# Kernel optimization log

Measured on AMD Instinct MI355X. Metric: run time of the kernel, lower is better.

Reference implementation:

```python
import jax, jax.numpy as jnp
import numpy as np

IN, H, B, T = 64, 256, 128, 512

def _uniform(key, shape, std):
    return jax.random.uniform(key, shape, jnp.float32, -std, std)

def setup_inputs() -> dict:
    key = jax.random.key(0)
    ks = jax.random.split(key, 16)
    std = 1.0 / np.sqrt(H)
    inp = {
        'x': jax.random.normal(ks[0], (B, T, IN), jnp.float32),
        # layer 1 sLSTM cell
        'Wxh1': _uniform(ks[1], (4 * H, IN), std), 'bxh1': _uniform(ks[2], (4 * H,), std),
        'Whh1': _uniform(ks[3], (4 * H, H), std),  'bhh1': _uniform(ks[4], (4 * H,), std),
        # layer 2 sLSTM cell
        'Wxh2': _uniform(ks[5], (4 * H, H), std),  'bxh2': _uniform(ks[6], (4 * H,), std),
        'Whh2': _uniform(ks[7], (4 * H, H), std),  'bhh2': _uniform(ks[8], (4 * H,), std),
        # head MLP
        'W1': _uniform(ks[9], (H // 2, H), 1.0 / np.sqrt(H)),      'b1': _uniform(ks[10], (H // 2,), 1.0 / np.sqrt(H)),
        'W2': _uniform(ks[11], (H // 4, H // 2), 1.0 / np.sqrt(H // 2)), 'b2': _uniform(ks[12], (H // 4,), 1.0 / np.sqrt(H // 2)),
        'W3': _uniform(ks[13], (1, H // 4), 1.0 / np.sqrt(H // 4)),      'b3': _uniform(ks[14], (1,), 1.0 / np.sqrt(H // 4)),
    }
    return inp

def _slstm_cell(x, h, c, m, n, Wxh, bxh, Whh, bhh):
    # gates: [B, 4H]
    gates = x @ Wxh.T + bxh + h @ Whh.T + bhh
    ig, fg, zg, og = jnp.split(gates, 4, axis=1)
    z_t = jnp.tanh(zg)
    o_t = jax.nn.sigmoid(og)
    # stabilizer: log(exp(fg)) = fg, log(exp(ig)) = ig
    m_t = jnp.maximum(fg + m, ig)
    i_t = jnp.exp(ig - m_t)
    f_t = jnp.exp(fg + m - m_t)
    c_t = f_t * c + i_t * z_t
    n_t = f_t * n + i_t
    h_t = o_t * (c_t / n_t)
    return h_t, c_t, m_t, n_t

def reference(x, Wxh1, bxh1, Whh1, bhh1, Wxh2, bxh2, Whh2, bhh2, W1, b1, W2, b2, W3, b3):
    Bq = x.shape[0]
    z = jnp.zeros((Bq, H), x.dtype)
    init = (z, z, z, z, z, z, z, z)  # (h1,c1,m1,n1,h2,c2,m2,n2)

    def step(carry, x_t):
        h1, c1, m1, n1, h2, c2, m2, n2 = carry
        h1, c1, m1, n1 = _slstm_cell(x_t, h1, c1, m1, n1, Wxh1, bxh1, Whh1, bhh1)
        h2, c2, m2, n2 = _slstm_cell(h1, h2, c2, m2, n2, Wxh2, bxh2, Whh2, bhh2)
        return (h1, c1, m1, n1, h2, c2, m2, n2), None

    carry, _ = jax.lax.scan(step, init, jnp.swapaxes(x, 0, 1))  # scan over time
    out = carry[4]  # last h2 == outputs[:, -1, :]
    out = jax.nn.relu(out @ W1.T + b1)   # dropout is identity in eval
    out = jax.nn.relu(out @ W2.T + b2)
    out = out @ W3.T + b3
    return out.squeeze(-1)  # [B]
```

## Files before the change

### kernel.cpp

```cpp
#include <hip/hip_runtime.h>
#include <stdint.h>

typedef unsigned short ushort_t;
typedef __attribute__((ext_vector_type(8))) short short8;
typedef __attribute__((ext_vector_type(4))) float float4v;
typedef __attribute__((ext_vector_type(4))) int int4v;

#define TSTEPS 512
#define NBATCH 128
#define HID 256
#define NIN 64
#define RB 32
#define NBHID (NBATCH*HID)

#define OFF_FLAGS   0u
#define OFF_BIAS    4096u
#define OFF_H1R     16384u
#define RING_BYTES  (RB*2u*NBATCH*HID*2u)
#define OFF_H2R     (OFF_H1R + RING_BYTES)
#define OFF_WF1     (OFF_H2R + RING_BYTES)
#define WF1_FRAGS   (16*8*4*4)
#define OFF_WF2     (OFF_WF1 + WF1_FRAGS*1024u)
#define WF2_FRAGS   (16*8*6*4)
#define OFF_HOUT    (OFF_WF2 + WF2_FRAGS*1024u)

__device__ __forceinline__ ushort_t bf16h(float f) {
    unsigned u = __float_as_uint(f);
    u += 0x7fffu + ((u >> 16) & 1u);
    return (ushort_t)(u >> 16);
}
__device__ __forceinline__ float bf16f(ushort_t h) {
    return __uint_as_float(((unsigned)h) << 16);
}


__device__ __forceinline__ int ld_cg_i32(const void* p) {
    int r;
    asm volatile("global_load_dword %0, %1, off sc0 sc1\n\ts_waitcnt vmcnt(0)"
                 : "=v"(r) : "v"(p) : "memory");
    return r;
}
__device__ __forceinline__ float ld_cg_f32(const void* p) {
    float r;
    asm volatile("global_load_dword %0, %1, off sc0 sc1\n\ts_waitcnt vmcnt(0)"
                 : "=v"(r) : "v"(p) : "memory");
    return r;
}
__device__ __forceinline__ void ld_cg_x2(int4v& a, int4v& b, const void* pa, const void* pb) {
    asm volatile("global_load_dwordx4 %0, %2, off sc0 sc1\n\t"
                 "global_load_dwordx4 %1, %3, off sc0 sc1\n\t"
                 "s_waitcnt vmcnt(0)"
                 : "=&v"(a), "=&v"(b)
                 : "v"(pa), "v"(pb) : "memory");
}
__device__ __forceinline__ void ld_cg_x4(int4v& a, int4v& b, int4v& c, int4v& d,
                                         const void* pa, const void* pb,
                                         const void* pc, const void* pd) {
    asm volatile("global_load_dwordx4 %0, %4, off sc0 sc1\n\t"
                 "global_load_dwordx4 %1, %5, off sc0 sc1\n\t"
                 "global_load_dwordx4 %2, %6, off sc0 sc1\n\t"
                 "global_load_dwordx4 %3, %7, off sc0 sc1\n\t"
                 "s_waitcnt vmcnt(0)"
                 : "=&v"(a), "=&v"(b), "=&v"(c), "=&v"(d)
                 : "v"(pa), "v"(pb), "v"(pc), "v"(pd) : "memory");
}
__device__ __forceinline__ void st_cg_u16(void* p, unsigned v) {
    asm volatile("global_store_short %0, %1, off sc0 sc1" :: "v"(p), "v"(v) : "memory");
}
__device__ __forceinline__ void st_cg_f32(void* p, float v) {
    asm volatile("global_store_dword %0, %1, off sc0 sc1" :: "v"(p), "v"(v) : "memory");
}
__device__ __forceinline__ void flag_release(void* p, int v) {
    asm volatile("s_waitcnt vmcnt(0)\n\tglobal_store_dword %0, %1, off sc0 sc1"
                 :: "v"(p), "v"(v) : "memory");
}


__global__ void prep_misc(const float* bxh1, const float* bhh1,
                          const float* bxh2, const float* bhh2,
                          float* bias, int* flags, ushort_t* h1r, ushort_t* h2r)
{
    int n = blockIdx.x * blockDim.x + threadIdx.x;
    if (n < 1024)       bias[n] = bxh1[n] + bhh1[n];
    else if (n < 2048)  bias[n] = bxh2[n - 1024] + bhh2[n - 1024];
    else if (n < 2304)  flags[n - 2048] = 0;
    else if (n < 2304 + 65536)  h1r[(RB-1)*2*NBHID + (n - 2304)] = 0;
    else if (n < 2304 + 131072) h2r[(RB-1)*2*NBHID + (n - 2304 - 65536)] = 0;
}

__global__ void prep_wf(const float* Wxh1, const float* Whh1,
                        const float* Wxh2, const float* Whh2,
                        ushort_t* wf1, ushort_t* wf2)
{
    int n = blockIdx.x * blockDim.x + threadIdx.x;
    const int L1E = WF1_FRAGS * 512;
    const int L2E = WF2_FRAGS * 512;
    if (n >= L1E + L2E) return;
    int layer = (n >= L1E) ? 1 : 0;
    int e = layer ? (n - L1E) : n;
    int el = e & 511;
    int f  = e >> 9;
    int lane = el >> 3, j = el & 7;
    int nt = f & 3;
    int rem = f >> 2;
    int i, wv, slice, F, S;
    if (!layer) { F = 4; S = 10; i = rem & 3; wv = (rem >> 2) & 7; slice = rem >> 5; }
    else        { F = 6; S = 16; i = rem % 6; int r2 = rem / 6; wv = r2 & 7; slice = r2 >> 3; }
    int fg = wv * F + i;
    int col = lane & 15;
    int row = nt * 256 + slice * 16 + col;
    float val = 0.f;
    if (fg < 3 * S) {
        int sec = (fg < S) ? 0 : ((fg < 2 * S) ? 1 : 2);
        int ks = (fg - sec * S) * 32 + (lane >> 4) * 8 + j;
        float w;
        if (!layer) w = (ks < 256) ? Whh1[row * 256 + ks] : Wxh1[row * 64 + (ks - 256)];
        else        w = (ks < 256) ? Wxh2[row * 256 + ks] : Whh2[row * 256 + (ks - 256)];
        ushort_t hi = bf16h(w);
        val = (sec < 2) ? bf16f(hi) : (w - bf16f(hi));
    }
    (layer ? wf2 : wf1)[e] = bf16h(val);
}


template<int LAYER, int F, int S, int PITCH>
__device__ __forceinline__ void run_layer(
    int g, int slice, int tid, const float* __restrict__ x,
    int* flags, const float* bias,
    ushort_t* h1r, ushort_t* h2r, const ushort_t* wfrag, float* hOut,
    ushort_t* sA, ushort_t* sB, float (*red)[4][64][4])
{
    const int wv = tid >> 6, lane = tid & 63;
    const int mrow = lane & 15, q = lane >> 4;
    int* f1 = flags + g * 16;
    int* f2 = flags + 128 + g * 16;
    int* myflag = flags + LAYER * 128 + g * 16 + slice;

    short8 bw[4][F];
    {
        const ushort_t* base = wfrag + (size_t)((slice * 8 + wv) * F) * 4 * 512;
        #pragma unroll
        for (int i = 0; i < F; i++)
            #pragma unroll
            for (int nt = 0; nt < 4; nt++)
                bw[nt][i] = *(const short8*)(base + (i * 4 + nt) * 512 + lane * 8);
    }

    float bs[4];
    #pragma unroll
    for (int nt = 0; nt < 4; nt++)
        bs[nt] = bias[LAYER * 1024 + nt * 256 + slice * 16 + mrow];

    float cst[4] = {0,0,0,0}, mst[4] = {0,0,0,0}, nst[4] = {0,0,0,0};

    for (int t = 0; t < TSTEPS; t++) {
        if (LAYER == 0 && tid >= 128 && tid < 256) {
            int idx = tid - 128;
            int r = idx >> 3, o = idx & 7;
            const float* xsrc = x + ((size_t)(g * 16 + r) * TSTEPS + t) * NIN + o * 8;
            float4v x0 = *(const float4v*)xsrc;
            float4v x1 = *(const float4v*)(xsrc + 4);
            float xs[8] = {x0[0], x0[1], x0[2], x0[3], x1[0], x1[1], x1[2], x1[3]};
            union { ushort_t u[8]; int4v v4; } hiP, loP;
            #pragma unroll
            for (int z = 0; z < 8; z++) {
                ushort_t hi = bf16h(xs[z]);
                hiP.u[z] = hi;
                loP.u[z] = bf16h(xs[z] - bf16f(hi));
            }
            *(int4v*)(sA + r * PITCH + (32 + o) * 8) = hiP.v4;
            *(int4v*)(sB + r * PITCH + (32 + o) * 8) = loP.v4;
        }

        if (tid < 64) {
            int* p = nullptr; int thr = 0;
            if (LAYER == 0) {
                if (lane < 16)      { p = f1 + lane;        thr = t; }
                else if (lane < 32) { p = f2 + (lane - 16); thr = t - 30; }
            } else {
                if (lane < 16)      { p = f1 + lane;        thr = t + 1; }
                else if (lane < 32) { p = f2 + (lane - 16); thr = t; }
            }
            if (p)
                while (ld_cg_i32(p) < thr) { }
        }
        __syncthreads();

        {
            int r = tid >> 5, k = tid & 31;
            int row = g * 16 + r;
            if (LAYER == 0) {
                int slot = (t - 1) & (RB - 1);
                const ushort_t* base = h1r + (size_t)slot * 2 * NBHID + (size_t)row * HID;
                const void* p0 = base + k * 8;
                const void* p1 = base + (size_t)NBHID + k * 8;
                int4v d0, d1;
                ld_cg_x2(d0, d1, p0, p1);
                *(int4v*)(sA + r * PITCH + k * 8) = d0;
                *(int4v*)(sB + r * PITCH + k * 8) = d1;
            } else {
                int s1 = t & (RB - 1), s2 = (t - 1) & (RB - 1);
                const ushort_t* b1h = h1r + (size_t)s1 * 2 * NBHID + (size_t)row * HID;
                const ushort_t* b2h = h2r + (size_t)s2 * 2 * NBHID + (size_t)row * HID;
                const void* p0 = b1h + k * 8;
                const void* p1 = b2h + k * 8;
                const void* p2 = b1h + (size_t)NBHID + k * 8;
                const void* p3 = b2h + (size_t)NBHID + k * 8;
                int4v d0, d1, d2, d3;
                ld_cg_x4(d0, d1, d2, d3, p0, p1, p2, p3);
                *(int4v*)(sA + r * PITCH + k * 8)        = d0;
                *(int4v*)(sA + r * PITCH + (32 + k) * 8) = d1;
                *(int4v*)(sB + r * PITCH + k * 8)        = d2;
                *(int4v*)(sB + r * PITCH + (32 + k) * 8) = d3;
            }
        }
        __syncthreads();

        float4v acc[4] = {};
        #pragma unroll
        for (int i = 0; i < F; i++) {
            const int fg = wv * F + i;
            short8 a;
            if (fg < 3 * S) {
                int sec = (fg >= S && fg < 2 * S) ? 1 : 0;
                int ks = ((fg < S) ? fg : ((fg < 2 * S) ? fg - S : fg - 2 * S)) * 32;
                const ushort_t* ap = (sec ? sB : sA) + mrow * PITCH + ks + q * 8;
                a = *(const short8*)ap;
            } else {
                a = (short8){0,0,0,0,0,0,0,0};
            }
            #pragma unroll
            for (int nt = 0; nt < 4; nt++)
                acc[nt] = __builtin_amdgcn_mfma_f32_16x16x32_bf16(a, bw[nt][i], acc[nt], 0, 0, 0);
        }

        if (wv >= 4) {
            #pragma unroll
            for (int nt = 0; nt < 4; nt++) *(float4v*)red[wv][nt][lane] = acc[nt];
        }
        __syncthreads();
        if (wv < 4) {
            #pragma unroll
            for (int nt = 0; nt < 4; nt++) acc[nt] += *(const float4v*)red[wv + 4][nt][lane];
            if (wv >= 2) {
                #pragma unroll
                for (int nt = 0; nt < 4; nt++) *(float4v*)red[wv][nt][lane] = acc[nt];
            }
        }
        __syncthreads();
        if (wv < 2) {
            #pragma unroll
            for (int nt = 0; nt < 4; nt++) acc[nt] += *(const float4v*)red[wv + 2][nt][lane];
            if (wv == 1) {
                #pragma unroll
                for (int nt = 0; nt < 4; nt++) *(float4v*)red[1][nt][lane] = acc[nt];
            }
        }
        __syncthreads();

        if (wv == 0) {
            #pragma unroll
            for (int nt = 0; nt < 4; nt++) acc[nt] += *(const float4v*)red[1][nt][lane];

            ushort_t* ring = LAYER ? h2r : h1r;
            int slotW = t & (RB - 1);
            #pragma unroll
            for (int r = 0; r < 4; r++) {
                float ig  = acc[0][r] + bs[0];
                float fgt = acc[1][r] + bs[1];
                float zg  = acc[2][r] + bs[2];
                float og  = acc[3][r] + bs[3];
                float zc = fminf(fmaxf(zg, -15.f), 15.f);
                float e2 = __expf(2.f * zc);
                float zt = (e2 - 1.f) / (e2 + 1.f);
                float ot = 1.f / (1.f + __expf(-og));
                float mt = fmaxf(fgt + mst[r], ig);
                float it = __expf(ig - mt);
                float ft = __expf(fgt + mst[r] - mt);
                cst[r] = ft * cst[r] + it * zt;
                nst[r] = ft * nst[r] + it;
                mst[r] = mt;
                float h = ot * (cst[r] / nst[r]);
                ushort_t hi = bf16h(h);
                ushort_t lo = bf16h(h - bf16f(hi));
                int row = g * 16 + q * 4 + r;
                int col = slice * 16 + mrow;
                st_cg_u16(ring + ((size_t)(slotW * 2 + 0) * NBATCH + row) * HID + col, (unsigned)hi);
                st_cg_u16(ring + ((size_t)(slotW * 2 + 1) * NBATCH + row) * HID + col, (unsigned)lo);
                if (LAYER == 1 && t == TSTEPS - 1)
                    st_cg_f32(hOut + (size_t)row * HID + col, h);
            }
            if (lane == 0)
                flag_release(myflag, t + 1);
        }
    }
}

__global__ __launch_bounds__(512, 2) void recur(
    const float* __restrict__ x,
    int* flags, const float* bias,
    ushort_t* h1r, ushort_t* h2r, const ushort_t* wf1, const ushort_t* wf2, float* hOut)
{
    __shared__ ushort_t sA[16 * 520];
    __shared__ ushort_t sB[16 * 520];
    __shared__ float red[8][4][64][4];
    int g = blockIdx.x & 7;
    int loc = blockIdx.x >> 3;
    if (loc < 16)
        run_layer<0, 4, 10, 328>(g, loc, threadIdx.x, x, flags, bias, h1r, h2r, wf1, hOut, sA, sB, red);
    else
        run_layer<1, 6, 16, 520>(g, loc - 16, threadIdx.x, x, flags, bias, h1r, h2r, wf2, hOut, sA, sB, red);
}


__global__ void head_mlp(const float* hOut, const float* W1, const float* b1,
                         const float* W2, const float* b2, const float* W3, const float* b3,
                         float* out)
{
    __shared__ float h[256];
    __shared__ float a1[128];
    __shared__ float a2[64];
    int b = blockIdx.x, j = threadIdx.x;
    for (int k = j; k < 256; k += 128)
        h[k] = ld_cg_f32(hOut + (size_t)b * HID + k);
    __syncthreads();
    float s = b1[j];
    for (int k = 0; k < 256; k++) s += W1[j * 256 + k] * h[k];
    a1[j] = fmaxf(s, 0.f);
    __syncthreads();
    if (j < 64) {
        float s2 = b2[j];
        for (int k = 0; k < 128; k++) s2 += W2[j * 128 + k] * a1[k];
        a2[j] = fmaxf(s2, 0.f);
    }
    __syncthreads();
    if (j == 0) {
        float s3 = b3[0];
        for (int k = 0; k < 64; k++) s3 += W3[k] * a2[k];
        out[b] = s3;
    }
}


extern "C" void kernel_launch(void* const* d_in, const int* in_sizes, int n_in,
                              void* d_out, int out_size, void* d_ws, size_t ws_size,
                              hipStream_t stream)
{
    const float* x    = (const float*)d_in[0];
    const float* Wxh1 = (const float*)d_in[1];
    const float* bxh1 = (const float*)d_in[2];
    const float* Whh1 = (const float*)d_in[3];
    const float* bhh1 = (const float*)d_in[4];
    const float* Wxh2 = (const float*)d_in[5];
    const float* bxh2 = (const float*)d_in[6];
    const float* Whh2 = (const float*)d_in[7];
    const float* bhh2 = (const float*)d_in[8];
    const float* W1   = (const float*)d_in[9];
    const float* b1   = (const float*)d_in[10];
    const float* W2   = (const float*)d_in[11];
    const float* b2   = (const float*)d_in[12];
    const float* W3   = (const float*)d_in[13];
    const float* b3   = (const float*)d_in[14];

    char* w = (char*)d_ws;
    int*      flags = (int*)(w + OFF_FLAGS);
    float*    bias  = (float*)(w + OFF_BIAS);
    ushort_t* h1r   = (ushort_t*)(w + OFF_H1R);
    ushort_t* h2r   = (ushort_t*)(w + OFF_H2R);
    ushort_t* wf1   = (ushort_t*)(w + OFF_WF1);
    ushort_t* wf2   = (ushort_t*)(w + OFF_WF2);
    float*    hOut  = (float*)(w + OFF_HOUT);

    prep_misc<<<(2304 + 131072 + 255) / 256, 256, 0, stream>>>(bxh1, bhh1, bxh2, bhh2,
                                                               bias, flags, h1r, h2r);
    prep_wf<<<((WF1_FRAGS + WF2_FRAGS) * 512 + 255) / 256, 256, 0, stream>>>(
        Wxh1, Whh1, Wxh2, Whh2, wf1, wf2);

    const float* xp = x;
    void* args[] = { (void*)&xp, (void*)&flags, (void*)&bias,
                     (void*)&h1r, (void*)&h2r, (void*)&wf1, (void*)&wf2, (void*)&hOut };
    hipLaunchCooperativeKernel((void*)recur, dim3(256), dim3(512), args, 0, stream);

    head_mlp<<<NBATCH, 128, 0, stream>>>(hOut, W1, b1, W2, b2, W3, b3, (float*)d_out);
}
```

Before: 1.983 ms.

## Replace per-step flag handshakes with generation-tagged ring entries

```diff
diff --git a/kernel.cpp b/kernel.cpp
--- a/kernel.cpp
+++ b/kernel.cpp
@@ -12,17 +12,19 @@
 #define NIN 64
 #define RB 32
 #define NBHID (NBATCH*HID)
+#define RING_DW (RB*NBHID)
 
 #define OFF_FLAGS   0u
 #define OFF_BIAS    4096u
 #define OFF_H1R     16384u
-#define RING_BYTES  (RB*2u*NBATCH*HID*2u)
+#define RING_BYTES  (RB*(unsigned)NBATCH*HID*4u)
 #define OFF_H2R     (OFF_H1R + RING_BYTES)
 #define OFF_WF1     (OFF_H2R + RING_BYTES)
 #define WF1_FRAGS   (16*8*4*4)
 #define OFF_WF2     (OFF_WF1 + WF1_FRAGS*1024u)
 #define WF2_FRAGS   (16*8*6*4)
 #define OFF_HOUT    (OFF_WF2 + WF2_FRAGS*1024u)
+
 
 __device__ __forceinline__ ushort_t bf16h(float f) {
     unsigned u = __float_as_uint(f);
@@ -64,28 +66,55 @@
                  : "=&v"(a), "=&v"(b), "=&v"(c), "=&v"(d)
                  : "v"(pa), "v"(pb), "v"(pc), "v"(pd) : "memory");
 }
-__device__ __forceinline__ void st_cg_u16(void* p, unsigned v) {
-    asm volatile("global_store_short %0, %1, off sc0 sc1" :: "v"(p), "v"(v) : "memory");
+__device__ __forceinline__ void st_cg_u32(void* p, unsigned v) {
+    asm volatile("global_store_dword %0, %1, off sc0 sc1" :: "v"(p), "v"(v) : "memory");
+}
+__device__ __forceinline__ void st_cg_i32(int* p, int v) {
+    asm volatile("global_store_dword %0, %1, off sc0 sc1" :: "v"(p), "v"(v) : "memory");
 }
 __device__ __forceinline__ void st_cg_f32(void* p, float v) {
     asm volatile("global_store_dword %0, %1, off sc0 sc1" :: "v"(p), "v"(v) : "memory");
 }
-__device__ __forceinline__ void flag_release(void* p, int v) {
-    asm volatile("s_waitcnt vmcnt(0)\n\tglobal_store_dword %0, %1, off sc0 sc1"
-                 :: "v"(p), "v"(v) : "memory");
+
+__device__ __forceinline__ bool tags8_ok(int4v a, int4v b, unsigned eg) {
+    return (((unsigned)a[0] & 31u) == eg) & (((unsigned)a[1] & 31u) == eg) &
+           (((unsigned)a[2] & 31u) == eg) & (((unsigned)a[3] & 31u) == eg) &
+           (((unsigned)b[0] & 31u) == eg) & (((unsigned)b[1] & 31u) == eg) &
+           (((unsigned)b[2] & 31u) == eg) & (((unsigned)b[3] & 31u) == eg);
+}
+
+__device__ __forceinline__ void emit_hilo8(int4v d0, int4v d1, ushort_t* pA, ushort_t* pB) {
+    union { ushort_t u[8]; int4v v4; } hiP, loP;
+    #pragma unroll
+    for (int z = 0; z < 8; z++) {
+        unsigned u = ((unsigned)(z < 4 ? d0[z] : d1[z - 4])) & ~31u;
+        float f = __uint_as_float(u);
+        ushort_t hi = bf16h(f);
+        hiP.u[z] = hi;
+        loP.u[z] = bf16h(f - bf16f(hi));
+    }
+    *(int4v*)pA = hiP.v4;
+    *(int4v*)pB = loP.v4;
 }
 
 
 __global__ void prep_misc(const float* bxh1, const float* bhh1,
                           const float* bxh2, const float* bhh2,
-                          float* bias, int* flags, ushort_t* h1r, ushort_t* h2r)
+                          float* bias, int* flags, unsigned* h1r, unsigned* h2r)
 {
     int n = blockIdx.x * blockDim.x + threadIdx.x;
     if (n < 1024)       bias[n] = bxh1[n] + bhh1[n];
     else if (n < 2048)  bias[n] = bxh2[n - 1024] + bhh2[n - 1024];
     else if (n < 2304)  flags[n - 2048] = 0;
-    else if (n < 2304 + 65536)  h1r[(RB-1)*2*NBHID + (n - 2304)] = 0;
-    else if (n < 2304 + 131072) h2r[(RB-1)*2*NBHID + (n - 2304 - 65536)] = 0;
+    else {
+        int d = n - 2304;
+        if (d < 2 * RING_DW) {
+            unsigned* ring = (d < RING_DW) ? h1r : h2r;
+            int e = (d < RING_DW) ? d : d - RING_DW;
+            int slot = e >> 15;
+            ring[e] = (slot == RB - 1) ? 0x1Fu : 0x10u;
+        }
+    }
 }
 
 __global__ void prep_wf(const float* Wxh1, const float* Whh1,
@@ -127,13 +156,13 @@
 __device__ __forceinline__ void run_layer(
     int g, int slice, int tid, const float* __restrict__ x,
     int* flags, const float* bias,
-    ushort_t* h1r, ushort_t* h2r, const ushort_t* wfrag, float* hOut,
+    unsigned* h1r, unsigned* h2r, const ushort_t* wfrag, float* hOut,
     ushort_t* sA, ushort_t* sB, float (*red)[4][64][4])
 {
     const int wv = tid >> 6, lane = tid & 63;
     const int mrow = lane & 15, q = lane >> 4;
-    int* f1 = flags + g * 16;
-    int* f2 = flags + 128 + g * 16;
+    int* p1 = flags + g * 16;
+    int* p2 = flags + 128 + g * 16;
     int* myflag = flags + LAYER * 128 + g * 16 + slice;
 
     short8 bw[4][F];
@@ -172,49 +201,51 @@
             *(int4v*)(sB + r * PITCH + (32 + o) * 8) = loP.v4;
         }
 
-        if (tid < 64) {
-            int* p = nullptr; int thr = 0;
+        if ((t & 7) == 0 && t >= 32 && tid < 64) {
+            int thr = t - 24;
+            int* p = nullptr;
             if (LAYER == 0) {
-                if (lane < 16)      { p = f1 + lane;        thr = t; }
-                else if (lane < 32) { p = f2 + (lane - 16); thr = t - 30; }
+                if (lane < 16)      p = p1 + lane;
+                else if (lane < 32) p = p2 + (lane - 16);
             } else {
-                if (lane < 16)      { p = f1 + lane;        thr = t + 1; }
-                else if (lane < 32) { p = f2 + (lane - 16); thr = t; }
+                if (lane < 16)      p = p2 + lane;
             }
             if (p)
                 while (ld_cg_i32(p) < thr) { }
         }
-        __syncthreads();
 
         {
             int r = tid >> 5, k = tid & 31;
             int row = g * 16 + r;
             if (LAYER == 0) {
                 int slot = (t - 1) & (RB - 1);
-                const ushort_t* base = h1r + (size_t)slot * 2 * NBHID + (size_t)row * HID;
-                const void* p0 = base + k * 8;
-                const void* p1 = base + (size_t)NBHID + k * 8;
+                unsigned eg = ((unsigned)(t - 1) >> 5) & 31u;
+                const unsigned* base = h1r + ((size_t)slot * NBATCH + row) * HID + k * 8;
                 int4v d0, d1;
-                ld_cg_x2(d0, d1, p0, p1);
-                *(int4v*)(sA + r * PITCH + k * 8) = d0;
-                *(int4v*)(sB + r * PITCH + k * 8) = d1;
+                for (;;) {
+                    ld_cg_x2(d0, d1, base, base + 4);
+                    if (tags8_ok(d0, d1, eg)) break;
+                }
+                emit_hilo8(d0, d1, sA + r * PITCH + k * 8, sB + r * PITCH + k * 8);
             } else {
                 int s1 = t & (RB - 1), s2 = (t - 1) & (RB - 1);
-                const ushort_t* b1h = h1r + (size_t)s1 * 2 * NBHID + (size_t)row * HID;
-                const ushort_t* b2h = h2r + (size_t)s2 * 2 * NBHID + (size_t)row * HID;
-                const void* p0 = b1h + k * 8;
-                const void* p1 = b2h + k * 8;
-                const void* p2 = b1h + (size_t)NBHID + k * 8;
-                const void* p3 = b2h + (size_t)NBHID + k * 8;
+                unsigned e1 = ((unsigned)t >> 5) & 31u;
+                unsigned e2 = ((unsigned)(t - 1) >> 5) & 31u;
+                const unsigned* b1 = h1r + ((size_t)s1 * NBATCH + row) * HID + k * 8;
+                const unsigned* b2 = h2r + ((size_t)s2 * NBATCH + row) * HID + k * 8;
                 int4v d0, d1, d2, d3;
-                ld_cg_x4(d0, d1, d2, d3, p0, p1, p2, p3);
-                *(int4v*)(sA + r * PITCH + k * 8)        = d0;
-                *(int4v*)(sA + r * PITCH + (32 + k) * 8) = d1;
-                *(int4v*)(sB + r * PITCH + k * 8)        = d2;
-                *(int4v*)(sB + r * PITCH + (32 + k) * 8) = d3;
+                for (;;) {
+                    ld_cg_x4(d0, d1, d2, d3, b1, b1 + 4, b2, b2 + 4);
+                    if (tags8_ok(d0, d1, e1) && tags8_ok(d2, d3, e2)) break;
+                }
+                emit_hilo8(d0, d1, sA + r * PITCH + k * 8,        sB + r * PITCH + k * 8);
+                emit_hilo8(d2, d3, sA + r * PITCH + (32 + k) * 8, sB + r * PITCH + (32 + k) * 8);
             }
         }
         __syncthreads();
+
+        if (tid == 0 && (t & 7) == 0)
+            st_cg_i32(myflag, t);
 
         float4v acc[4] = {};
         #pragma unroll
@@ -262,8 +293,9 @@
             #pragma unroll
             for (int nt = 0; nt < 4; nt++) acc[nt] += *(const float4v*)red[1][nt][lane];
 
-            ushort_t* ring = LAYER ? h2r : h1r;
+            unsigned* ring = LAYER ? h2r : h1r;
             int slotW = t & (RB - 1);
+            unsigned gen = (unsigned)t >> 5;
             #pragma unroll
             for (int r = 0; r < 4; r++) {
                 float ig  = acc[0][r] + bs[0];
@@ -281,17 +313,14 @@
                 nst[r] = ft * nst[r] + it;
                 mst[r] = mt;
                 float h = ot * (cst[r] / nst[r]);
-                ushort_t hi = bf16h(h);
-                ushort_t lo = bf16h(h - bf16f(hi));
                 int row = g * 16 + q * 4 + r;
                 int col = slice * 16 + mrow;
-                st_cg_u16(ring + ((size_t)(slotW * 2 + 0) * NBATCH + row) * HID + col, (unsigned)hi);
-                st_cg_u16(ring + ((size_t)(slotW * 2 + 1) * NBATCH + row) * HID + col, (unsigned)lo);
+                unsigned uh = __float_as_uint(h);
+                uh = ((uh + 16u) & ~31u) | gen;
+                st_cg_u32(ring + ((size_t)slotW * NBATCH + row) * HID + col, uh);
                 if (LAYER == 1 && t == TSTEPS - 1)
                     st_cg_f32(hOut + (size_t)row * HID + col, h);
             }
-            if (lane == 0)
-                flag_release(myflag, t + 1);
         }
     }
 }
@@ -299,7 +328,7 @@
 __global__ __launch_bounds__(512, 2) void recur(
     const float* __restrict__ x,
     int* flags, const float* bias,
-    ushort_t* h1r, ushort_t* h2r, const ushort_t* wf1, const ushort_t* wf2, float* hOut)
+    unsigned* h1r, unsigned* h2r, const ushort_t* wf1, const ushort_t* wf2, float* hOut)
 {
     __shared__ ushort_t sA[16 * 520];
     __shared__ ushort_t sB[16 * 520];
@@ -365,14 +394,14 @@
     char* w = (char*)d_ws;
     int*      flags = (int*)(w + OFF_FLAGS);
     float*    bias  = (float*)(w + OFF_BIAS);
-    ushort_t* h1r   = (ushort_t*)(w + OFF_H1R);
-    ushort_t* h2r   = (ushort_t*)(w + OFF_H2R);
+    unsigned* h1r   = (unsigned*)(w + OFF_H1R);
+    unsigned* h2r   = (unsigned*)(w + OFF_H2R);
     ushort_t* wf1   = (ushort_t*)(w + OFF_WF1);
     ushort_t* wf2   = (ushort_t*)(w + OFF_WF2);
     float*    hOut  = (float*)(w + OFF_HOUT);
 
-    prep_misc<<<(2304 + 131072 + 255) / 256, 256, 0, stream>>>(bxh1, bhh1, bxh2, bhh2,
-                                                               bias, flags, h1r, h2r);
+    prep_misc<<<(2304 + 2 * RING_DW + 255) / 256, 256, 0, stream>>>(bxh1, bhh1, bxh2, bhh2,
+                                                                    bias, flags, h1r, h2r);
     prep_wf<<<((WF1_FRAGS + WF2_FRAGS) * 512 + 255) / 256, 256, 0, stream>>>(
         Wxh1, Whh1, Wxh2, Whh2, wf1, wf2);
 
```

Result: slower. 2.838 ms (+43.1%).
